# Kernel optimization log

Measured on AMD Instinct MI355X. Metric: run time of the kernel, lower is better.

## Reference

```python
import jax, jax.numpy as jnp
import numpy as np

B, S, E, H = 4, 2048, 1024, 16
D = E // H  # head dim


def setup_inputs() -> dict:
    key = jax.random.key(0)
    ks = jax.random.split(key, 6)
    sc = 1.0 / np.sqrt(E)
    return {
        "x":  jax.random.normal(ks[0], (B, S, E), dtype=jnp.float32),
        "Wk": jax.random.normal(ks[1], (E, E), dtype=jnp.float32) * sc,
        "Wq": jax.random.normal(ks[2], (E, E), dtype=jnp.float32) * sc,
        "Wv": jax.random.normal(ks[3], (E, E), dtype=jnp.float32) * sc,
        "Wo": jax.random.normal(ks[4], (E, E), dtype=jnp.float32) * sc,
        "bo": jax.random.normal(ks[5], (E,), dtype=jnp.float32) * sc,
    }


def reference(x, Wk, Wq, Wv, Wo, bo):
    b, s, e = x.shape
    # torch Linear: y = x @ W.T (weights are [out, in])
    K = x @ Wk.T
    Q = x @ Wq.T
    _V_unused = x @ Wv.T  # computed in source but discarded (V = Q.view bug)
    # split heads: [b, s, H, D] -> [b, H, s, D]
    Kh = K.reshape(b, s, H, D).transpose(0, 2, 1, 3)
    Qh = Q.reshape(b, s, H, D).transpose(0, 2, 1, 3)
    Vh = Qh  # faithful to source: V = Q.view(...)
    # scaled dot product, scaled by sqrt(embedding_size) as in source
    scores = jnp.einsum('bhqd,bhkd->bhqk', Qh, Kh) / jnp.sqrt(jnp.float32(e))
    causal = jnp.tril(jnp.ones((s, s), dtype=bool))
    scores = jnp.where(causal, scores, -jnp.inf)
    probs = jax.nn.softmax(scores, axis=-1)
    attn = jnp.einsum('bhqk,bhkd->bhqd', probs, Vh)
    attn = attn.transpose(0, 2, 1, 3).reshape(b, s, e)
    return attn @ Wo.T + bo
```

## Files before the change

kernel.cpp:

```cpp
#include <hip/hip_runtime.h>
#include <hip/hip_bf16.h>

#define PB 4
#define PS 2048
#define PE 1024
#define PH 16
#define PD 64

typedef __attribute__((ext_vector_type(8))) short bf16x8;
typedef __attribute__((ext_vector_type(4))) float f32x4;
typedef const __attribute__((address_space(1))) unsigned int* gas_t;
typedef __attribute__((address_space(3))) unsigned int* las_t;

__device__ __forceinline__ unsigned short f2bf(float f) {
  union { float f; unsigned int u; } v;
  v.f = f;
  unsigned int u = v.u;
  u += 0x7fffu + ((u >> 16) & 1u);
  return (unsigned short)(u >> 16);
}

__device__ __forceinline__ f32x4 mfma16(bf16x8 a, bf16x8 b, f32x4 c) {
  return __builtin_amdgcn_mfma_f32_16x16x32_bf16(a, b, c, 0, 0, 0);
}

#define CVT_GROUPS ((PB * PS * PE + 3 * PE * PE) / 4)
#define CVT_BLOCKS (CVT_GROUPS / 256)
__global__ __launch_bounds__(256) void cvt_kernel(
    const float* __restrict__ x, const float* __restrict__ wk,
    const float* __restrict__ wq, const float* __restrict__ wo,
    unsigned short* __restrict__ xb, unsigned short* __restrict__ wkb,
    unsigned short* __restrict__ wqb, unsigned short* __restrict__ wob) {
  const long long NX = (long long)PB * PS * PE;
  const long long NW = (long long)PE * PE;
  long long i = ((long long)blockIdx.x * 256 + threadIdx.x) * 4;
  const float* src;
  unsigned short* dst;
  long long off;
  if (i < NX)               { src = x;  dst = xb;  off = i; }
  else if (i < NX + NW)     { src = wk; dst = wkb; off = i - NX; }
  else if (i < NX + 2 * NW) { src = wq; dst = wqb; off = i - NX - NW; }
  else                      { src = wo; dst = wob; off = i - NX - 2 * NW; }
  float4 v = *(const float4*)(src + off);
  ushort4 o;
  o.x = f2bf(v.x); o.y = f2bf(v.y); o.z = f2bf(v.z); o.w = f2bf(v.w);
  *(ushort4*)(dst + off) = o;
}

__global__ __launch_bounds__(256) void gemm_qk(
    const unsigned short* __restrict__ A, const unsigned short* __restrict__ Bq,
    const unsigned short* __restrict__ Bk,
    unsigned short* __restrict__ QT, unsigned short* __restrict__ Kb) {
  const int K = PE, N = PE;
  __shared__ __attribute__((aligned(16))) unsigned short As[128 * 64];
  __shared__ __attribute__((aligned(16))) unsigned short Bqs[128 * 64];
  __shared__ __attribute__((aligned(16))) unsigned short Bks[128 * 64];
  const int tid = threadIdx.x;
  const int wave = tid >> 6, lane = tid & 63;
  const int quad = lane >> 4, ln = lane & 15;
  const int m0 = blockIdx.y * 128, n0 = blockIdx.x * 128;
  const int wm = (wave >> 1) * 64, wn = (wave & 1) * 64;

  f32x4 aq[4][4], ak[4][4];
#pragma unroll
  for (int i = 0; i < 4; ++i)
#pragma unroll
    for (int j = 0; j < 4; ++j)
#pragma unroll
      for (int r = 0; r < 4; ++r) { aq[i][j][r] = 0.f; ak[i][j][r] = 0.f; }

  for (int k0 = 0; k0 < K; k0 += 64) {
#pragma unroll
    for (int it = 0; it < 4; ++it) {
      const int idx = it * 256 + tid;
      const int row = idx >> 3, ch = idx & 7;
      const int gch = ch ^ (row & 7);
      __builtin_amdgcn_global_load_lds(
          (gas_t)(const void*)(A + (size_t)(m0 + row) * K + k0 + gch * 8),
          (las_t)(void*)((char*)As + idx * 16), 16, 0, 0);
      __builtin_amdgcn_global_load_lds(
          (gas_t)(const void*)(Bq + (size_t)(n0 + row) * K + k0 + gch * 8),
          (las_t)(void*)((char*)Bqs + idx * 16), 16, 0, 0);
      __builtin_amdgcn_global_load_lds(
          (gas_t)(const void*)(Bk + (size_t)(n0 + row) * K + k0 + gch * 8),
          (las_t)(void*)((char*)Bks + idx * 16), 16, 0, 0);
    }
    __syncthreads();
#pragma unroll
    for (int kc = 0; kc < 2; ++kc) {
      bf16x8 af[4], bqf[4], bkf[4];
#pragma unroll
      for (int t = 0; t < 4; ++t) {
        const int ra = wm + t * 16 + ln;
        const int rb = wn + t * 16 + ln;
        af[t]  = *(const bf16x8*)(As  + ra * 64 + ((kc * 4 + quad) ^ (ra & 7)) * 8);
        bqf[t] = *(const bf16x8*)(Bqs + rb * 64 + ((kc * 4 + quad) ^ (rb & 7)) * 8);
        bkf[t] = *(const bf16x8*)(Bks + rb * 64 + ((kc * 4 + quad) ^ (rb & 7)) * 8);
      }
#pragma unroll
      for (int mt = 0; mt < 4; ++mt)
#pragma unroll
        for (int nt = 0; nt < 4; ++nt) {
          aq[mt][nt] = mfma16(af[mt], bqf[nt], aq[mt][nt]);
          ak[mt][nt] = mfma16(af[mt], bkf[nt], ak[mt][nt]);
        }
    }
    __syncthreads();
  }

  const float CEXP = 0.045084220f;
#pragma unroll
  for (int mt = 0; mt < 4; ++mt) {
#pragma unroll
    for (int nt = 0; nt < 4; ++nt) {
      const int row = m0 + wm + mt * 16 + quad * 4;
      const int col = n0 + wn + nt * 16 + ln;
      const int b = row >> 11, s = row & 2047;
      const int h = col >> 6, d = col & 63;
      ushort4 ov;
      ov.x = f2bf(aq[mt][nt][0]); ov.y = f2bf(aq[mt][nt][1]);
      ov.z = f2bf(aq[mt][nt][2]); ov.w = f2bf(aq[mt][nt][3]);
      *(ushort4*)(QT + (((size_t)(b * PH + h) * PD + d) * PS + s)) = ov;
#pragma unroll
      for (int r = 0; r < 4; ++r)
        Kb[(size_t)(row + r) * N + col] = f2bf(ak[mt][nt][r] * CEXP);
    }
  }
}

__global__ __launch_bounds__(256) void gemm_out(
    const unsigned short* __restrict__ A, const unsigned short* __restrict__ Bm,
    const float* __restrict__ bias, float* __restrict__ Cf) {
  const int K = PE, N = PE;
  __shared__ __attribute__((aligned(16))) unsigned short As[128 * 64];
  __shared__ __attribute__((aligned(16))) unsigned short Bs[128 * 64];
  const int tid = threadIdx.x;
  const int wave = tid >> 6, lane = tid & 63;
  const int quad = lane >> 4, ln = lane & 15;
  const int m0 = blockIdx.y * 128, n0 = blockIdx.x * 128;
  const int wm = (wave >> 1) * 64, wn = (wave & 1) * 64;

  f32x4 acc[4][4];
#pragma unroll
  for (int i = 0; i < 4; ++i)
#pragma unroll
    for (int j = 0; j < 4; ++j)
#pragma unroll
      for (int r = 0; r < 4; ++r) acc[i][j][r] = 0.f;

  for (int k0 = 0; k0 < K; k0 += 64) {
#pragma unroll
    for (int it = 0; it < 4; ++it) {
      const int idx = it * 256 + tid;
      const int row = idx >> 3, ch = idx & 7;
      const int gch = ch ^ (row & 7);
      __builtin_amdgcn_global_load_lds(
          (gas_t)(const void*)(A + (size_t)(m0 + row) * K + k0 + gch * 8),
          (las_t)(void*)((char*)As + idx * 16), 16, 0, 0);
      __builtin_amdgcn_global_load_lds(
          (gas_t)(const void*)(Bm + (size_t)(n0 + row) * K + k0 + gch * 8),
          (las_t)(void*)((char*)Bs + idx * 16), 16, 0, 0);
    }
    __syncthreads();
#pragma unroll
    for (int kc = 0; kc < 2; ++kc) {
      bf16x8 af[4], bfr[4];
#pragma unroll
      for (int t = 0; t < 4; ++t) {
        const int ra = wm + t * 16 + ln;
        const int rb = wn + t * 16 + ln;
        af[t]  = *(const bf16x8*)(As + ra * 64 + ((kc * 4 + quad) ^ (ra & 7)) * 8);
        bfr[t] = *(const bf16x8*)(Bs + rb * 64 + ((kc * 4 + quad) ^ (rb & 7)) * 8);
      }
#pragma unroll
      for (int mt = 0; mt < 4; ++mt)
#pragma unroll
        for (int nt = 0; nt < 4; ++nt)
          acc[mt][nt] = mfma16(af[mt], bfr[nt], acc[mt][nt]);
    }
    __syncthreads();
  }

#pragma unroll
  for (int mt = 0; mt < 4; ++mt) {
#pragma unroll
    for (int nt = 0; nt < 4; ++nt) {
      const int row = m0 + wm + mt * 16 + quad * 4;
      const int col = n0 + wn + nt * 16 + ln;
      const float bv = bias[col];
#pragma unroll
      for (int r = 0; r < 4; ++r)
        Cf[(size_t)(row + r) * N + col] = acc[mt][nt][r] + bv;
    }
  }
}

__global__ __launch_bounds__(256) void attn_kernel(
    const unsigned short* __restrict__ QT,
    const unsigned short* __restrict__ Kb,
    unsigned short* __restrict__ Ab) {
  __shared__ __attribute__((aligned(16))) unsigned short Ks[64 * 64];
  __shared__ __attribute__((aligned(16))) unsigned short Vs[64 * 64];
  __shared__ __attribute__((aligned(16))) unsigned short Ps[4][16 * 72];

  const int tid = threadIdx.x;
  const int wave = tid >> 6, lane = tid & 63;
  const int quad = lane >> 4, ln = lane & 15;
  const int h = blockIdx.y, b = blockIdx.z;
  const size_t hoff  = ((size_t)b * PS) * PE + (size_t)h * PD;
  const size_t hofft = ((size_t)(b * PH + h) * PD) * PS;
  const int srow = tid >> 3, sch = tid & 7;

  for (int pass = 0; pass < 2; ++pass) {
    const int qc = pass ? (int)blockIdx.x : 31 - (int)blockIdx.x;
    const int qw0 = qc * 64 + wave * 16;

    bf16x8 qfr[2];
#pragma unroll
    for (int c = 0; c < 2; ++c) {
      union { unsigned short u[8]; bf16x8 v; } tmp;
#pragma unroll
      for (int j = 0; j < 8; ++j)
        tmp.u[j] = QT[hofft + (size_t)(c * 32 + quad * 8 + j) * PS + qw0 + ln];
      qfr[c] = tmp.v;
    }

    f32x4 o[4];
    float psum = 0.f;
#pragma unroll
    for (int td = 0; td < 4; ++td)
#pragma unroll
      for (int r = 0; r < 4; ++r) o[td][r] = 0.f;

    const int ktend = qc + 1;
    for (int kt = 0; kt < ktend; ++kt) {
      const int k0 = kt * 64;

#pragma unroll
      for (int r = 0; r < 2; ++r) {
        const int row = r * 32 + srow;
        const int gch = sch ^ (row & 7);
        __builtin_amdgcn_global_load_lds(
            (gas_t)(const void*)(Kb + hoff + (size_t)(k0 + row) * PE + gch * 8),
            (las_t)(void*)((char*)Ks + (r * 256 + tid) * 16), 16, 0, 0);
        __builtin_amdgcn_global_load_lds(
            (gas_t)(const void*)(QT + hofft + (size_t)row * PS + k0 + gch * 8),
            (las_t)(void*)((char*)Vs + (r * 256 + tid) * 16), 16, 0, 0);
      }
      __syncthreads();

      f32x4 sacc[4];
#pragma unroll
      for (int mk = 0; mk < 4; ++mk)
#pragma unroll
        for (int r = 0; r < 4; ++r) sacc[mk][r] = 0.f;
#pragma unroll
      for (int c = 0; c < 2; ++c) {
        const int ch = ((c * 4 + quad) ^ (ln & 7)) * 8;
        bf16x8 kf[4];
#pragma unroll
        for (int mk = 0; mk < 4; ++mk)
          kf[mk] = *(const bf16x8*)(Ks + (mk * 16 + ln) * 64 + ch);
#pragma unroll
        for (int mk = 0; mk < 4; ++mk)
          sacc[mk] = mfma16(kf[mk], qfr[c], sacc[mk]);
      }

      const bool edge = (k0 + 63) > qw0;
#pragma unroll
      for (int mk = 0; mk < 4; ++mk) {
        float p[4];
#pragma unroll
        for (int r = 0; r < 4; ++r)
          p[r] = __builtin_amdgcn_exp2f(sacc[mk][r]);
        if (edge) {
          const int qg = qw0 + ln;
#pragma unroll
          for (int r = 0; r < 4; ++r) {
            const int kg = k0 + mk * 16 + quad * 4 + r;
            p[r] = (kg <= qg) ? p[r] : 0.f;
          }
        }
        psum += (p[0] + p[1]) + (p[2] + p[3]);
        union { __hip_bfloat162 h2; unsigned int u; } u01, u23;
        u01.h2 = __float22bfloat162_rn(float2{p[0], p[1]});
        u23.h2 = __float22bfloat162_rn(float2{p[2], p[3]});
        *(uint2*)(&Ps[wave][ln * 72 + mk * 16 + quad * 4]) =
            uint2{u01.u, u23.u};
      }

#pragma unroll
      for (int c = 0; c < 2; ++c) {
        const int ch = ((c * 4 + quad) ^ (ln & 7)) * 8;
        bf16x8 pf = *(const bf16x8*)(&Ps[wave][ln * 72 + c * 32 + quad * 8]);
#pragma unroll
        for (int td = 0; td < 4; ++td) {
          bf16x8 vfd = *(const bf16x8*)(Vs + (td * 16 + ln) * 64 + ch);
          o[td] = mfma16(pf, vfd, o[td]);
        }
      }
      __syncthreads();
    }

    psum += __shfl_xor(psum, 16, 64);
    psum += __shfl_xor(psum, 32, 64);
    float invq[4];
#pragma unroll
    for (int r = 0; r < 4; ++r)
      invq[r] = 1.f / __shfl(psum, quad * 4 + r, 64);

#pragma unroll
    for (int r = 0; r < 4; ++r) {
      const int qg = qw0 + quad * 4 + r;
#pragma unroll
      for (int td = 0; td < 4; ++td)
        Ab[hoff + (size_t)qg * PE + td * 16 + ln] =
            f2bf(o[td][r] * invq[r]);
    }
  }
}

extern "C" void kernel_launch(void* const* d_in, const int* in_sizes, int n_in,
                              void* d_out, int out_size, void* d_ws, size_t ws_size,
                              hipStream_t stream) {
  (void)in_sizes; (void)n_in; (void)out_size; (void)ws_size;
  const float* x  = (const float*)d_in[0];
  const float* Wk = (const float*)d_in[1];
  const float* Wq = (const float*)d_in[2];
  const float* Wo = (const float*)d_in[4];
  const float* bo = (const float*)d_in[5];
  float* out = (float*)d_out;

  char* ws = (char*)d_ws;
  unsigned short* xb  = (unsigned short*)(ws);
  unsigned short* wkb = (unsigned short*)(ws + (16u << 20));
  unsigned short* wqb = (unsigned short*)(ws + (18u << 20));
  unsigned short* wob = (unsigned short*)(ws + (20u << 20));
  unsigned short* QT  = (unsigned short*)(ws + (22u << 20));
  unsigned short* Kb  = (unsigned short*)(ws + (38u << 20));
  unsigned short* Ab  = xb;

  const int M = PB * PS;

  cvt_kernel<<<dim3(CVT_BLOCKS), dim3(256), 0, stream>>>(
      x, Wk, Wq, Wo, xb, wkb, wqb, wob);

  gemm_qk<<<dim3(PE / 128, M / 128), dim3(256), 0, stream>>>(
      xb, wqb, wkb, QT, Kb);

  attn_kernel<<<dim3(16, PH, PB), dim3(256), 0, stream>>>(QT, Kb, Ab);

  gemm_out<<<dim3(PE / 128, M / 128), dim3(256), 0, stream>>>(
      Ab, wob, bo, out);
}
```

Before: 257.9 us.

## Double-buffer K tiles in LDS and load V fragments directly from global

The K tile in shared memory is now double-buffered: the next tile is prefetched while the current one is consumed, which leaves one barrier per iteration instead of a load-then-sync step. The V tile (from the transposed Q) is no longer staged in LDS; each wave reads its MFMA fragments straight from global memory into registers. s_setprio is raised around the MFMA sections. This aims to hide global load latency and cut LDS traffic, at the cost of more registers and redundant, less coalesced global reads of V across waves.

```diff
diff --git a/kernel.cpp b/kernel.cpp
--- a/kernel.cpp
+++ b/kernel.cpp
@@ -199,8 +199,7 @@
     const unsigned short* __restrict__ QT,
     const unsigned short* __restrict__ Kb,
     unsigned short* __restrict__ Ab) {
-  __shared__ __attribute__((aligned(16))) unsigned short Ks[64 * 64];
-  __shared__ __attribute__((aligned(16))) unsigned short Vs[64 * 64];
+  __shared__ __attribute__((aligned(16))) unsigned short Ks[2][64 * 64];
   __shared__ __attribute__((aligned(16))) unsigned short Ps[4][16 * 72];
 
   const int tid = threadIdx.x;
@@ -211,6 +210,7 @@
   const size_t hofft = ((size_t)(b * PH + h) * PD) * PS;
   const int srow = tid >> 3, sch = tid & 7;
 
+  int cur = 0;
   for (int pass = 0; pass < 2; ++pass) {
     const int qc = pass ? (int)blockIdx.x : 31 - (int)blockIdx.x;
     const int qw0 = qc * 64 + wave * 16;
@@ -225,6 +225,16 @@
       qfr[c] = tmp.v;
     }
 
+#pragma unroll
+    for (int r = 0; r < 2; ++r) {
+      const int row = r * 32 + srow;
+      const int gch = sch ^ (row & 7);
+      __builtin_amdgcn_global_load_lds(
+          (gas_t)(const void*)(Kb + hoff + (size_t)row * PE + gch * 8),
+          (las_t)(void*)((char*)&Ks[cur][0] + (r * 256 + tid) * 16), 16, 0, 0);
+    }
+    __syncthreads();
+
     f32x4 o[4];
     float psum = 0.f;
 #pragma unroll
@@ -236,35 +246,46 @@
     for (int kt = 0; kt < ktend; ++kt) {
       const int k0 = kt * 64;
 
-#pragma unroll
-      for (int r = 0; r < 2; ++r) {
-        const int row = r * 32 + srow;
-        const int gch = sch ^ (row & 7);
-        __builtin_amdgcn_global_load_lds(
-            (gas_t)(const void*)(Kb + hoff + (size_t)(k0 + row) * PE + gch * 8),
-            (las_t)(void*)((char*)Ks + (r * 256 + tid) * 16), 16, 0, 0);
-        __builtin_amdgcn_global_load_lds(
-            (gas_t)(const void*)(QT + hofft + (size_t)row * PS + k0 + gch * 8),
-            (las_t)(void*)((char*)Vs + (r * 256 + tid) * 16), 16, 0, 0);
-      }
-      __syncthreads();
-
+      if (kt + 1 < ktend) {
+        const int nk0 = k0 + 64;
+#pragma unroll
+        for (int r = 0; r < 2; ++r) {
+          const int row = r * 32 + srow;
+          const int gch = sch ^ (row & 7);
+          __builtin_amdgcn_global_load_lds(
+              (gas_t)(const void*)(Kb + hoff + (size_t)(nk0 + row) * PE + gch * 8),
+              (las_t)(void*)((char*)&Ks[cur ^ 1][0] + (r * 256 + tid) * 16),
+              16, 0, 0);
+        }
+      }
+
+      bf16x8 vf[2][4];
+#pragma unroll
+      for (int c = 0; c < 2; ++c)
+#pragma unroll
+        for (int td = 0; td < 4; ++td)
+          vf[c][td] = *(const bf16x8*)(QT + hofft +
+              (size_t)(td * 16 + ln) * PS + k0 + (c * 4 + quad) * 8);
+
+      const unsigned short* kcur = &Ks[cur][0];
       f32x4 sacc[4];
 #pragma unroll
       for (int mk = 0; mk < 4; ++mk)
 #pragma unroll
         for (int r = 0; r < 4; ++r) sacc[mk][r] = 0.f;
+      __builtin_amdgcn_s_setprio(1);
 #pragma unroll
       for (int c = 0; c < 2; ++c) {
         const int ch = ((c * 4 + quad) ^ (ln & 7)) * 8;
         bf16x8 kf[4];
 #pragma unroll
         for (int mk = 0; mk < 4; ++mk)
-          kf[mk] = *(const bf16x8*)(Ks + (mk * 16 + ln) * 64 + ch);
+          kf[mk] = *(const bf16x8*)(kcur + (mk * 16 + ln) * 64 + ch);
 #pragma unroll
         for (int mk = 0; mk < 4; ++mk)
           sacc[mk] = mfma16(kf[mk], qfr[c], sacc[mk]);
       }
+      __builtin_amdgcn_s_setprio(0);
 
       const bool edge = (k0 + 63) > qw0;
 #pragma unroll
@@ -289,17 +310,18 @@
             uint2{u01.u, u23.u};
       }
 
+      __builtin_amdgcn_s_setprio(1);
 #pragma unroll
       for (int c = 0; c < 2; ++c) {
-        const int ch = ((c * 4 + quad) ^ (ln & 7)) * 8;
         bf16x8 pf = *(const bf16x8*)(&Ps[wave][ln * 72 + c * 32 + quad * 8]);
 #pragma unroll
-        for (int td = 0; td < 4; ++td) {
-          bf16x8 vfd = *(const bf16x8*)(Vs + (td * 16 + ln) * 64 + ch);
-          o[td] = mfma16(pf, vfd, o[td]);
-        }
-      }
+        for (int td = 0; td < 4; ++td)
+          o[td] = mfma16(pf, vf[c][td], o[td]);
+      }
+      __builtin_amdgcn_s_setprio(0);
+
       __syncthreads();
+      cur ^= 1;
     }
 
     psum += __shfl_xor(psum, 16, 64);
```

Measured after the change: 354.7 us. +37.5%, slower.
